# Kernel optimization log

Hardware: AMD Instinct MI355X
Metric: run time of the kernel (lower is better)

The kernel has to match this reference:

```python
import jax, jax.numpy as jnp
import numpy as np

B, T, E, D = 8, 2048, 1024, 64  # batch, seq_len, n_emb, head_dim

def setup_inputs() -> dict:
    key = jax.random.key(0)
    ks = jax.random.split(key, 4)
    scale = 1.0 / np.sqrt(E)
    return {
        "x": jax.random.normal(ks[0], (B, T, E), dtype=jnp.float32),
        "Wq": jax.random.normal(ks[1], (E, D), dtype=jnp.float32) * scale,
        "bq": jnp.zeros((D,), dtype=jnp.float32),
        "Wk": jax.random.normal(ks[2], (E, D), dtype=jnp.float32) * scale,
        "bk": jnp.zeros((D,), dtype=jnp.float32),
        "Wv": jax.random.normal(ks[3], (E, D), dtype=jnp.float32) * scale,
        "bv": jnp.zeros((D,), dtype=jnp.float32),
    }

def reference(x, Wq, bq, Wk, bk, Wv, bv):
    # QKV projections: [B,T,E] @ [E,D] -> [B,T,D]
    q = x @ Wq + bq
    k = x @ Wk + bk
    v = x @ Wv + bv
    d = q.shape[-1]
    # scaled dot-product scores [B,T,T]
    wei = jnp.einsum('btd,bsd->bts', q, k) * (d ** -0.5)
    # causal mask: position t attends to s <= t
    t = wei.shape[1]
    causal = jnp.tril(jnp.ones((t, t), dtype=bool))
    wei = jnp.where(causal, wei, -jnp.inf)
    wei = jax.nn.softmax(wei, axis=-1)
    # attention output [B,T,D]
    return jnp.einsum('bts,bsd->btd', wei, v)
```

## Files before the change

### kernel.cpp

```cpp
#include <hip/hip_runtime.h>
#include <math.h>


#define B_   8
#define T_   2048
#define E_   1024
#define D_   64
#define BT_  (B_ * T_)

typedef __attribute__((ext_vector_type(8))) short s16x8;
typedef __attribute__((ext_vector_type(4))) short s16x4;
typedef __attribute__((ext_vector_type(4))) float f32x4;

__device__ __forceinline__ short f2bf(float f) {
    union { float f; unsigned u; } a; a.f = f;
    unsigned r = a.u + 0x7fffu + ((a.u >> 16) & 1u);
    return (short)(r >> 16);
}

#define MFMA16(a, b, c) __builtin_amdgcn_mfma_f32_16x16x32_bf16((a), (b), (c), 0, 0, 0)

#define DPPF(x, ctrl) __builtin_bit_cast(float, \
    __builtin_amdgcn_update_dpp(0, __builtin_bit_cast(int, (x)), (ctrl), 0xF, 0xF, true))

__device__ __forceinline__ float rsum16(float x) {
    x += DPPF(x, 0xB1);
    x += DPPF(x, 0x4E);
    x += DPPF(x, 0x124);
    x += DPPF(x, 0x128);
    return x;
}

__global__ __launch_bounds__(256) void wtrans_kernel(
    const float* __restrict__ Wq, const float* __restrict__ Wk,
    const float* __restrict__ Wv, short* __restrict__ Wt)
{
    __shared__ float sT[64][65];
    const int sel = blockIdx.x >> 4;
    const int k0  = (blockIdx.x & 15) * 64;
    const float* W = sel == 0 ? Wq : (sel == 1 ? Wk : Wv);
    const int t  = threadIdx.x;
    const int kr = t >> 4, c4 = (t & 15) * 4;
    #pragma unroll
    for (int i = 0; i < 4; ++i) {
        float4 v = *(const float4*)&W[(size_t)(k0 + kr + i * 16) * D_ + c4];
        sT[kr + i * 16][c4 + 0] = v.x; sT[kr + i * 16][c4 + 1] = v.y;
        sT[kr + i * 16][c4 + 2] = v.z; sT[kr + i * 16][c4 + 3] = v.w;
    }
    __syncthreads();
    #pragma unroll
    for (int i = 0; i < 4; ++i) {
        int n  = (t >> 4) + i * 16;
        int kk = (t & 15) * 4;
        s16x4 o;
        o.x = f2bf(sT[kk + 0][n]); o.y = f2bf(sT[kk + 1][n]);
        o.z = f2bf(sT[kk + 2][n]); o.w = f2bf(sT[kk + 3][n]);
        *(s16x4*)&Wt[(size_t)(sel * 64 + n) * E_ + k0 + kk] = o;
    }
}

__global__ __launch_bounds__(512) void qkv_kernel(
    const float* __restrict__ x, const short* __restrict__ Wt,
    const float* __restrict__ bq, const float* __restrict__ bk,
    const float* __restrict__ bv,
    short* __restrict__ Qg, short* __restrict__ Kg, short* __restrict__ VTg)
{
    __shared__ short sX[2][64 * 140];
    const int tid  = threadIdx.x;
    const int lane = tid & 63;
    const int w    = tid >> 6;
    const int l15  = lane & 15, quad = lane >> 4;
    const int h2   = w & 1;
    const int n2   = w >> 1;
    const int t0   = blockIdx.x * 64;
    const int bb   = t0 >> 11;

    const int srow = tid >> 3;
    const int skc  = (tid & 7) * 16;
    const float* px = &x[(size_t)(t0 + srow) * E_ + skc];

    f32x4 acc[3][2];
    #pragma unroll
    for (int a = 0; a < 3; ++a)
        #pragma unroll
        for (int h = 0; h < 2; ++h)
            acc[a][h] = (f32x4){0.f, 0.f, 0.f, 0.f};

    float4 lda0 = *(const float4*)(px +   0);
    float4 lda1 = *(const float4*)(px +   4);
    float4 lda2 = *(const float4*)(px +   8);
    float4 lda3 = *(const float4*)(px +  12);
    float4 ldb0 = *(const float4*)(px + 128);
    float4 ldb1 = *(const float4*)(px + 132);
    float4 ldb2 = *(const float4*)(px + 136);
    float4 ldb3 = *(const float4*)(px + 140);

    int buf = 0;
    for (int k0 = 0; k0 < E_; k0 += 128) {
        s16x8 pk0, pk1;
        pk0[0] = f2bf(lda0.x); pk0[1] = f2bf(lda0.y);
        pk0[2] = f2bf(lda0.z); pk0[3] = f2bf(lda0.w);
        pk0[4] = f2bf(lda1.x); pk0[5] = f2bf(lda1.y);
        pk0[6] = f2bf(lda1.z); pk0[7] = f2bf(lda1.w);
        pk1[0] = f2bf(lda2.x); pk1[1] = f2bf(lda2.y);
        pk1[2] = f2bf(lda2.z); pk1[3] = f2bf(lda2.w);
        pk1[4] = f2bf(lda3.x); pk1[5] = f2bf(lda3.y);
        pk1[6] = f2bf(lda3.z); pk1[7] = f2bf(lda3.w);
        *(s16x8*)&sX[buf][srow * 140 + skc]     = pk0;
        *(s16x8*)&sX[buf][srow * 140 + skc + 8] = pk1;
        __syncthreads();

        lda0 = ldb0; lda1 = ldb1; lda2 = ldb2; lda3 = ldb3;
        if (k0 + 256 < E_) {
            const float* p2 = px + k0 + 256;
            ldb0 = *(const float4*)(p2 +  0);
            ldb1 = *(const float4*)(p2 +  4);
            ldb2 = *(const float4*)(p2 +  8);
            ldb3 = *(const float4*)(p2 + 12);
        }

        s16x8 aw[3][4];
        #pragma unroll
        for (int t3 = 0; t3 < 3; ++t3) {
            const short* pw = &Wt[(size_t)((n2 * 3 + t3) * 16 + l15) * E_ + k0 + quad * 8];
            #pragma unroll
            for (int kc = 0; kc < 4; ++kc)
                aw[t3][kc] = *(const s16x8*)(pw + kc * 32);
        }
        s16x8 bxf[2][4];
        #pragma unroll
        for (int h = 0; h < 2; ++h) {
            const int trow = (h2 * 2 + h) * 16 + l15;
            #pragma unroll
            for (int kc = 0; kc < 4; ++kc)
                bxf[h][kc] = *(const s16x8*)&sX[buf][trow * 140 + kc * 32 + quad * 8];
        }
        #pragma unroll
        for (int t3 = 0; t3 < 3; ++t3)
            #pragma unroll
            for (int h = 0; h < 2; ++h)
                #pragma unroll
                for (int kc = 0; kc < 4; ++kc)
                    acc[t3][h] = MFMA16(aw[t3][kc], bxf[h][kc], acc[t3][h]);
        buf ^= 1;
    }

    __syncthreads();
    short* sVT = &sX[0][0];

    #pragma unroll
    for (int t3 = 0; t3 < 3; ++t3) {
        const int nt = n2 * 3 + t3;
        const int fb = (nt & 3) * 16 + quad * 4;
        const float* bias = nt < 4 ? bq : (nt < 8 ? bk : bv);
        f32x4 bsv = *(const f32x4*)&bias[fb];
        #pragma unroll
        for (int h = 0; h < 2; ++h) {
            const int lt  = (h2 * 2 + h) * 16 + l15;
            const int tok = t0 + lt;
            f32x4 v = acc[t3][h] + bsv;
            if (nt < 4) {
                v *= 0.125f;
                s16x4 o = { f2bf(v[0]), f2bf(v[1]), f2bf(v[2]), f2bf(v[3]) };
                *(s16x4*)&Qg[(size_t)tok * D_ + fb] = o;
            } else if (nt < 8) {
                s16x4 o = { f2bf(v[0]), f2bf(v[1]), f2bf(v[2]), f2bf(v[3]) };
                *(s16x4*)&Kg[(size_t)tok * D_ + fb] = o;
            } else {
                #pragma unroll
                for (int r = 0; r < 4; ++r)
                    sVT[(fb + r) * 72 + lt] = f2bf(v[r]);
            }
        }
    }
    __syncthreads();
    {
        const int d  = tid >> 3;
        const int tq = (tid & 7) * 8;
        s16x8 vv = *(const s16x8*)&sVT[d * 72 + tq];
        *(s16x8*)&VTg[(size_t)(bb * D_ + d) * T_ + (t0 & (T_ - 1)) + tq] = vv;
    }
}

__global__ __launch_bounds__(256) void attn_kernel(
    const short* __restrict__ Qg, const short* __restrict__ Kg,
    const short* __restrict__ VTg, float* __restrict__ out)
{
    __shared__ char smem[20736];
    short* sP = (short*)smem;
    float* sO = (float*)smem;
    float* sl = (float*)(smem + 20480);

    const int tid  = threadIdx.x;
    const int lane = tid & 63;
    const int w    = tid >> 6;
    const int l15  = lane & 15, quad = lane >> 4;
    const int b    = blockIdx.x & 7;
    const int pr   = blockIdx.x >> 3;
    const int jA   = pr, jB = 127 - pr;
    const int tqA  = jA * 16, tqB = jB * 16;
    const int nchA = (jA >> 2) + 1, nchB = (jB >> 2) + 1;
    const int tot  = nchA + nchB;
    const int seg  = (tot + 3) >> 2;
    const int c0   = w * seg;
    const int c1   = (c0 + seg < tot) ? c0 + seg : tot;

    const size_t qoffA = ((size_t)b * T_ + tqA + l15) * D_ + quad * 8;
    const s16x8 aqA0 = *(const s16x8*)&Qg[qoffA];
    const s16x8 aqA1 = *(const s16x8*)&Qg[qoffA + 32];
    const size_t qoffB = ((size_t)b * T_ + tqB + l15) * D_ + quad * 8;
    const s16x8 aqB0 = *(const s16x8*)&Qg[qoffB];
    const s16x8 aqB1 = *(const s16x8*)&Qg[qoffB + 32];

    f32x4 oA[4], oB[4];
    float lA[4] = {0.f, 0.f, 0.f, 0.f}, lB[4] = {0.f, 0.f, 0.f, 0.f};
    #pragma unroll
    for (int nt = 0; nt < 4; ++nt) {
        oA[nt] = (f32x4){0.f, 0.f, 0.f, 0.f};
        oB[nt] = (f32x4){0.f, 0.f, 0.f, 0.f};
    }

    const short* kb = Kg  + (size_t)b * T_ * D_;
    const short* vb = VTg + (size_t)b * D_ * T_;
    short* sPw = sP + w * (16 * 72);

    auto body = [&](int cc, int tq, int nch, const s16x8& q0, const s16x8& q1,
                    f32x4 (&oo)[4], float (&lp)[4]) {
        const int s0 = cc * 64;
        s16x8 bk[4][2];
        #pragma unroll
        for (int nt = 0; nt < 4; ++nt) {
            const short* pk = kb + (size_t)(s0 + nt * 16 + l15) * D_ + quad * 8;
            bk[nt][0] = *(const s16x8*)pk;
            bk[nt][1] = *(const s16x8*)(pk + 32);
        }
        const f32x4 zz = (f32x4){0.f, 0.f, 0.f, 0.f};
        f32x4 sacc[4];
        #pragma unroll
        for (int nt = 0; nt < 4; ++nt) {
            sacc[nt] = MFMA16(q0, bk[nt][0], zz);
            sacc[nt] = MFMA16(q1, bk[nt][1], sacc[nt]);
        }
        s16x8 bv[4][2];
        #pragma unroll
        for (int nt = 0; nt < 4; ++nt) {
            const short* pv = vb + (size_t)(nt * 16 + l15) * T_ + s0 + quad * 8;
            bv[nt][0] = *(const s16x8*)pv;
            bv[nt][1] = *(const s16x8*)(pv + 32);
        }
        const bool diag = (cc == nch - 1);
        float p[4][4];
        #pragma unroll
        for (int nt = 0; nt < 4; ++nt)
            #pragma unroll
            for (int r = 0; r < 4; ++r) {
                float e = __expf(sacc[nt][r]);
                if (diag && (s0 + nt * 16 + l15 > tq + quad * 4 + r)) e = 0.f;
                p[nt][r] = e;
            }
        #pragma unroll
        for (int r = 0; r < 4; ++r)
            lp[r] += (p[0][r] + p[1][r]) + (p[2][r] + p[3][r]);
        #pragma unroll
        for (int nt = 0; nt < 4; ++nt)
            #pragma unroll
            for (int r = 0; r < 4; ++r)
                sPw[(quad * 4 + r) * 72 + nt * 16 + l15] = f2bf(p[nt][r]);
        s16x8 ap0 = *(const s16x8*)&sPw[l15 * 72 + quad * 8];
        s16x8 ap1 = *(const s16x8*)&sPw[l15 * 72 + 32 + quad * 8];
        #pragma unroll
        for (int nt = 0; nt < 4; ++nt) {
            oo[nt] = MFMA16(ap0, bv[nt][0], oo[nt]);
            oo[nt] = MFMA16(ap1, bv[nt][1], oo[nt]);
        }
    };

    const int aEnd   = (c1 < nchA) ? c1 : nchA;
    const int bStart = (c0 > nchA) ? c0 : nchA;
    for (int c = c0; c < aEnd; ++c)
        body(c, tqA, nchA, aqA0, aqA1, oA, lA);
    for (int c = bStart; c < c1; ++c)
        body(c - nchA, tqB, nchB, aqB0, aqB1, oB, lB);

    f32x4 lvA, lvB;
    #pragma unroll
    for (int r = 0; r < 4; ++r) { lvA[r] = rsum16(lA[r]); lvB[r] = rsum16(lB[r]); }

    const int d  = tid & 63;
    const int rb = (tid >> 6) * 4;

    __syncthreads();
    {
        float* sOw = sO + w * (64 * 20);
        #pragma unroll
        for (int nt = 0; nt < 4; ++nt)
            *(f32x4*)&sOw[(nt * 16 + l15) * 20 + quad * 4] = oA[nt];
        if (l15 == 0) *(f32x4*)&sl[w * 16 + quad * 4] = lvA;
    }
    __syncthreads();
    {
        f32x4 osum = (f32x4){0.f, 0.f, 0.f, 0.f};
        f32x4 lsum = (f32x4){0.f, 0.f, 0.f, 0.f};
        #pragma unroll
        for (int w2 = 0; w2 < 4; ++w2) {
            osum += *(const f32x4*)&sO[w2 * (64 * 20) + d * 20 + rb];
            lsum += *(const f32x4*)&sl[w2 * 16 + rb];
        }
        #pragma unroll
        for (int i = 0; i < 4; ++i)
            out[((size_t)b * T_ + tqA + rb + i) * D_ + d] = osum[i] / lsum[i];
    }

    __syncthreads();
    {
        float* sOw = sO + w * (64 * 20);
        #pragma unroll
        for (int nt = 0; nt < 4; ++nt)
            *(f32x4*)&sOw[(nt * 16 + l15) * 20 + quad * 4] = oB[nt];
        if (l15 == 0) *(f32x4*)&sl[w * 16 + quad * 4] = lvB;
    }
    __syncthreads();
    {
        f32x4 osum = (f32x4){0.f, 0.f, 0.f, 0.f};
        f32x4 lsum = (f32x4){0.f, 0.f, 0.f, 0.f};
        #pragma unroll
        for (int w2 = 0; w2 < 4; ++w2) {
            osum += *(const f32x4*)&sO[w2 * (64 * 20) + d * 20 + rb];
            lsum += *(const f32x4*)&sl[w2 * 16 + rb];
        }
        #pragma unroll
        for (int i = 0; i < 4; ++i)
            out[((size_t)b * T_ + tqB + rb + i) * D_ + d] = osum[i] / lsum[i];
    }
}

extern "C" void kernel_launch(void* const* d_in, const int* in_sizes, int n_in,
                              void* d_out, int out_size, void* d_ws, size_t ws_size,
                              hipStream_t stream) {
    (void)in_sizes; (void)n_in; (void)out_size; (void)ws_size;
    const float* x  = (const float*)d_in[0];
    const float* Wq = (const float*)d_in[1];
    const float* bq = (const float*)d_in[2];
    const float* Wk = (const float*)d_in[3];
    const float* bk = (const float*)d_in[4];
    const float* Wv = (const float*)d_in[5];
    const float* bv = (const float*)d_in[6];

    char* ws = (char*)d_ws;
    short* Qg  = (short*)(ws);
    short* Kg  = (short*)(ws + (size_t)2 * 1024 * 1024);
    short* VTg = (short*)(ws + (size_t)4 * 1024 * 1024);
    short* Wt  = (short*)(ws + (size_t)6 * 1024 * 1024);

    wtrans_kernel<<<48, 256, 0, stream>>>(Wq, Wk, Wv, Wt);
    qkv_kernel<<<BT_ / 64, 512, 0, stream>>>(x, Wt, bq, bk, bv, Qg, Kg, VTg);
    attn_kernel<<<B_ * 64, 256, 0, stream>>>(Qg, Kg, VTg, (float*)d_out);
}
```

Before: 156.4 us.

## Process 32 contiguous query rows per block with 8 waves sharing K/V loads

Each attention block handled two paired 16-row query tiles (j and 127-j) split over 4 waves. It now handles 32 contiguous query rows with 8 waves. Every wave computes both 16-row tiles against each 64-key chunk, so each K/V fragment load feeds twice as many MFMAs. Shared memory for the cross-wave reduction grows to about 73 KB. The paired-tile load balancing is dropped, so per-block work now ranges from 1 to 32 chunks and higher LDS use may lower occupancy.

```diff
diff --git a/kernel.cpp b/kernel.cpp
--- a/kernel.cpp
+++ b/kernel.cpp
@@ -182,50 +182,50 @@
     }
 }
 
-__global__ __launch_bounds__(256) void attn_kernel(
+__global__ __launch_bounds__(512) void attn_kernel(
     const short* __restrict__ Qg, const short* __restrict__ Kg,
     const short* __restrict__ VTg, float* __restrict__ out)
 {
-    __shared__ char smem[20736];
+    __shared__ char smem[74752];
     short* sP = (short*)smem;
     float* sO = (float*)smem;
-    float* sl = (float*)(smem + 20480);
+    float* sl = (float*)(smem + 73728);
 
     const int tid  = threadIdx.x;
     const int lane = tid & 63;
     const int w    = tid >> 6;
     const int l15  = lane & 15, quad = lane >> 4;
     const int b    = blockIdx.x & 7;
-    const int pr   = blockIdx.x >> 3;
-    const int jA   = pr, jB = 127 - pr;
-    const int tqA  = jA * 16, tqB = jB * 16;
-    const int nchA = (jA >> 2) + 1, nchB = (jB >> 2) + 1;
-    const int tot  = nchA + nchB;
-    const int seg  = (tot + 3) >> 2;
-    const int c0   = w * seg;
-    const int c1   = (c0 + seg < tot) ? c0 + seg : tot;
-
-    const size_t qoffA = ((size_t)b * T_ + tqA + l15) * D_ + quad * 8;
-    const s16x8 aqA0 = *(const s16x8*)&Qg[qoffA];
-    const s16x8 aqA1 = *(const s16x8*)&Qg[qoffA + 32];
-    const size_t qoffB = ((size_t)b * T_ + tqB + l15) * D_ + quad * 8;
-    const s16x8 aqB0 = *(const s16x8*)&Qg[qoffB];
-    const s16x8 aqB1 = *(const s16x8*)&Qg[qoffB + 32];
-
-    f32x4 oA[4], oB[4];
-    float lA[4] = {0.f, 0.f, 0.f, 0.f}, lB[4] = {0.f, 0.f, 0.f, 0.f};
-    #pragma unroll
-    for (int nt = 0; nt < 4; ++nt) {
-        oA[nt] = (f32x4){0.f, 0.f, 0.f, 0.f};
-        oB[nt] = (f32x4){0.f, 0.f, 0.f, 0.f};
+    const int j    = blockIdx.x >> 3;
+    const int tq   = j * 32;
+    const int nch  = (j >> 1) + 1;
+    const int c0   = (w * nch) >> 3;
+    const int c1   = ((w + 1) * nch) >> 3;
+
+    s16x8 aq[2][2];
+    #pragma unroll
+    for (int qt = 0; qt < 2; ++qt) {
+        const size_t qoff = ((size_t)b * T_ + tq + qt * 16 + l15) * D_ + quad * 8;
+        aq[qt][0] = *(const s16x8*)&Qg[qoff];
+        aq[qt][1] = *(const s16x8*)&Qg[qoff + 32];
+    }
+
+    f32x4 oo[2][4];
+    float lp[2][4];
+    #pragma unroll
+    for (int qt = 0; qt < 2; ++qt) {
+        #pragma unroll
+        for (int nt = 0; nt < 4; ++nt)
+            oo[qt][nt] = (f32x4){0.f, 0.f, 0.f, 0.f};
+        #pragma unroll
+        for (int r = 0; r < 4; ++r) lp[qt][r] = 0.f;
     }
 
     const short* kb = Kg  + (size_t)b * T_ * D_;
     const short* vb = VTg + (size_t)b * D_ * T_;
-    short* sPw = sP + w * (16 * 72);
-
-    auto body = [&](int cc, int tq, int nch, const s16x8& q0, const s16x8& q1,
-                    f32x4 (&oo)[4], float (&lp)[4]) {
+    short* sPw = sP + w * (2 * 16 * 72);
+
+    for (int cc = c0; cc < c1; ++cc) {
         const int s0 = cc * 64;
         s16x8 bk[4][2];
         #pragma unroll
@@ -235,12 +235,14 @@
             bk[nt][1] = *(const s16x8*)(pk + 32);
         }
         const f32x4 zz = (f32x4){0.f, 0.f, 0.f, 0.f};
-        f32x4 sacc[4];
-        #pragma unroll
-        for (int nt = 0; nt < 4; ++nt) {
-            sacc[nt] = MFMA16(q0, bk[nt][0], zz);
-            sacc[nt] = MFMA16(q1, bk[nt][1], sacc[nt]);
-        }
+        f32x4 sacc[2][4];
+        #pragma unroll
+        for (int qt = 0; qt < 2; ++qt)
+            #pragma unroll
+            for (int nt = 0; nt < 4; ++nt) {
+                sacc[qt][nt] = MFMA16(aq[qt][0], bk[nt][0], zz);
+                sacc[qt][nt] = MFMA16(aq[qt][1], bk[nt][1], sacc[qt][nt]);
+            }
         s16x8 bv[4][2];
         #pragma unroll
         for (int nt = 0; nt < 4; ++nt) {
@@ -249,88 +251,77 @@
             bv[nt][1] = *(const s16x8*)(pv + 32);
         }
         const bool diag = (cc == nch - 1);
-        float p[4][4];
-        #pragma unroll
-        for (int nt = 0; nt < 4; ++nt)
-            #pragma unroll
-            for (int r = 0; r < 4; ++r) {
-                float e = __expf(sacc[nt][r]);
-                if (diag && (s0 + nt * 16 + l15 > tq + quad * 4 + r)) e = 0.f;
-                p[nt][r] = e;
+        float p[2][4][4];
+        #pragma unroll
+        for (int qt = 0; qt < 2; ++qt)
+            #pragma unroll
+            for (int nt = 0; nt < 4; ++nt)
+                #pragma unroll
+                for (int r = 0; r < 4; ++r) {
+                    float e = __expf(sacc[qt][nt][r]);
+                    if (diag && (s0 + nt * 16 + l15 > tq + qt * 16 + quad * 4 + r))
+                        e = 0.f;
+                    p[qt][nt][r] = e;
+                }
+        #pragma unroll
+        for (int qt = 0; qt < 2; ++qt)
+            #pragma unroll
+            for (int r = 0; r < 4; ++r)
+                lp[qt][r] += (p[qt][0][r] + p[qt][1][r]) + (p[qt][2][r] + p[qt][3][r]);
+        #pragma unroll
+        for (int qt = 0; qt < 2; ++qt)
+            #pragma unroll
+            for (int nt = 0; nt < 4; ++nt)
+                #pragma unroll
+                for (int r = 0; r < 4; ++r)
+                    sPw[qt * (16 * 72) + (quad * 4 + r) * 72 + nt * 16 + l15] =
+                        f2bf(p[qt][nt][r]);
+        #pragma unroll
+        for (int qt = 0; qt < 2; ++qt) {
+            s16x8 ap0 = *(const s16x8*)&sPw[qt * (16 * 72) + l15 * 72 + quad * 8];
+            s16x8 ap1 = *(const s16x8*)&sPw[qt * (16 * 72) + l15 * 72 + 32 + quad * 8];
+            #pragma unroll
+            for (int nt = 0; nt < 4; ++nt) {
+                oo[qt][nt] = MFMA16(ap0, bv[nt][0], oo[qt][nt]);
+                oo[qt][nt] = MFMA16(ap1, bv[nt][1], oo[qt][nt]);
             }
+        }
+    }
+
+    f32x4 lv[2];
+    #pragma unroll
+    for (int qt = 0; qt < 2; ++qt)
         #pragma unroll
         for (int r = 0; r < 4; ++r)
-            lp[r] += (p[0][r] + p[1][r]) + (p[2][r] + p[3][r]);
-        #pragma unroll
-        for (int nt = 0; nt < 4; ++nt)
-            #pragma unroll
-            for (int r = 0; r < 4; ++r)
-                sPw[(quad * 4 + r) * 72 + nt * 16 + l15] = f2bf(p[nt][r]);
-        s16x8 ap0 = *(const s16x8*)&sPw[l15 * 72 + quad * 8];
-        s16x8 ap1 = *(const s16x8*)&sPw[l15 * 72 + 32 + quad * 8];
-        #pragma unroll
-        for (int nt = 0; nt < 4; ++nt) {
-            oo[nt] = MFMA16(ap0, bv[nt][0], oo[nt]);
-            oo[nt] = MFMA16(ap1, bv[nt][1], oo[nt]);
-        }
-    };
-
-    const int aEnd   = (c1 < nchA) ? c1 : nchA;
-    const int bStart = (c0 > nchA) ? c0 : nchA;
-    for (int c = c0; c < aEnd; ++c)
-        body(c, tqA, nchA, aqA0, aqA1, oA, lA);
-    for (int c = bStart; c < c1; ++c)
-        body(c - nchA, tqB, nchB, aqB0, aqB1, oB, lB);
-
-    f32x4 lvA, lvB;
-    #pragma unroll
-    for (int r = 0; r < 4; ++r) { lvA[r] = rsum16(lA[r]); lvB[r] = rsum16(lB[r]); }
-
-    const int d  = tid & 63;
-    const int rb = (tid >> 6) * 4;
+            lv[qt][r] = rsum16(lp[qt][r]);
 
     __syncthreads();
     {
-        float* sOw = sO + w * (64 * 20);
-        #pragma unroll
-        for (int nt = 0; nt < 4; ++nt)
-            *(f32x4*)&sOw[(nt * 16 + l15) * 20 + quad * 4] = oA[nt];
-        if (l15 == 0) *(f32x4*)&sl[w * 16 + quad * 4] = lvA;
+        float* sOw = sO + w * (64 * 36);
+        #pragma unroll
+        for (int qt = 0; qt < 2; ++qt)
+            #pragma unroll
+            for (int nt = 0; nt < 4; ++nt)
+                *(f32x4*)&sOw[(nt * 16 + l15) * 36 + qt * 16 + quad * 4] = oo[qt][nt];
+        if (l15 == 0) {
+            *(f32x4*)&sl[w * 32 + quad * 4]      = lv[0];
+            *(f32x4*)&sl[w * 32 + 16 + quad * 4] = lv[1];
+        }
     }
     __syncthreads();
     {
+        const int d  = tid & 63;
+        const int rb = (tid >> 6) * 4;
         f32x4 osum = (f32x4){0.f, 0.f, 0.f, 0.f};
         f32x4 lsum = (f32x4){0.f, 0.f, 0.f, 0.f};
         #pragma unroll
-        for (int w2 = 0; w2 < 4; ++w2) {
-            osum += *(const f32x4*)&sO[w2 * (64 * 20) + d * 20 + rb];
-            lsum += *(const f32x4*)&sl[w2 * 16 + rb];
+        for (int w2 = 0; w2 < 8; ++w2) {
+            osum += *(const f32x4*)&sO[w2 * (64 * 36) + d * 36 + rb];
+            lsum += *(const f32x4*)&sl[w2 * 32 + rb];
         }
         #pragma unroll
         for (int i = 0; i < 4; ++i)
-            out[((size_t)b * T_ + tqA + rb + i) * D_ + d] = osum[i] / lsum[i];
-    }
-
-    __syncthreads();
-    {
-        float* sOw = sO + w * (64 * 20);
-        #pragma unroll
-        for (int nt = 0; nt < 4; ++nt)
-            *(f32x4*)&sOw[(nt * 16 + l15) * 20 + quad * 4] = oB[nt];
-        if (l15 == 0) *(f32x4*)&sl[w * 16 + quad * 4] = lvB;
-    }
-    __syncthreads();
-    {
-        f32x4 osum = (f32x4){0.f, 0.f, 0.f, 0.f};
-        f32x4 lsum = (f32x4){0.f, 0.f, 0.f, 0.f};
-        #pragma unroll
-        for (int w2 = 0; w2 < 4; ++w2) {
-            osum += *(const f32x4*)&sO[w2 * (64 * 20) + d * 20 + rb];
-            lsum += *(const f32x4*)&sl[w2 * 16 + rb];
-        }
-        #pragma unroll
-        for (int i = 0; i < 4; ++i)
-            out[((size_t)b * T_ + tqB + rb + i) * D_ + d] = osum[i] / lsum[i];
+            out[((size_t)b * T_ + tq + rb + i) * D_ + d] = osum[i] / lsum[i];
     }
 }
 
@@ -354,5 +345,5 @@
 
     wtrans_kernel<<<48, 256, 0, stream>>>(Wq, Wk, Wv, Wt);
     qkv_kernel<<<BT_ / 64, 512, 0, stream>>>(x, Wt, bq, bk, bv, Qg, Kg, VTg);
-    attn_kernel<<<B_ * 64, 256, 0, stream>>>(Qg, Kg, VTg, (float*)d_out);
-}
+    attn_kernel<<<B_ * 64, 512, 0, stream>>>(Qg, Kg, VTg, (float*)d_out);
+}
```

Result: faster. 151.7 us (-3.0%).
